# Kernel optimization log

Hardware: AMD Instinct MI355X
Metric: run time of the kernel (lower is better)

The kernel has to match this reference:

```python
import jax, jax.numpy as jnp
import numpy as np

B, NV, RN, SN = 1, 4, 1024, 128
H = W = 256
C_FEAT = 32   # img_feat_dim
D_VIEW = 32   # view transformer d_model
PE_D = 8      # PE_d_hid
D_RAY = D_VIEW + PE_D  # 40
NHEAD = 8
EPS_LN = 1e-5


def _layernorm(x, g, b):
    m = x.mean(-1, keepdims=True)
    v = ((x - m) ** 2).mean(-1, keepdims=True)
    return (x - m) * jax.lax.rsqrt(v + EPS_LN) * g + b


def _linear_attention(q, k, v):
    # LoFTR kernelized linear attention; q,k,v: (n, L, h, d)
    Q = jax.nn.elu(q) + 1.0
    K = jax.nn.elu(k) + 1.0
    L = v.shape[1]
    KV = jnp.einsum('nshd,nshv->nhdv', K, v / L)
    Z = 1.0 / (jnp.einsum('nlhd,nhd->nlh', Q, K.sum(axis=1)) + 1e-6)
    return jnp.einsum('nlhd,nhdv,nlh->nlhv', Q, KV, Z) * L


def _loftr_self_layer(x, Wq, Wk, Wv, Wm, g1, b1, W1, W2, g2, b2):
    # LoFTREncoderLayer with self-attention (x is both query and source)
    n, L, d = x.shape
    dim = d // NHEAD
    q = (x @ Wq).reshape(n, L, NHEAD, dim)
    k = (x @ Wk).reshape(n, L, NHEAD, dim)
    v = (x @ Wv).reshape(n, L, NHEAD, dim)
    msg = _linear_attention(q, k, v).reshape(n, L, d) @ Wm
    msg = _layernorm(msg, g1, b1)
    msg = jax.nn.relu(jnp.concatenate([x, msg], -1) @ W1) @ W2
    msg = _layernorm(msg, g2, b2)
    return x + msg


def _grid_sample_2d(img, pix):
    # img: (N,C,H,W); pix: (N,RN,SN,2) in pixel coords.
    # bilinear, align_corners=True, zero padding; mask = in-bounds.
    N, C, Hh, Ww = img.shape
    x, y = pix[..., 0], pix[..., 1]
    mask = ((x >= 0) & (x <= Ww - 1) & (y >= 0) & (y <= Hh - 1)).astype(img.dtype)
    x0 = jnp.floor(x)
    y0 = jnp.floor(y)
    flat = img.reshape(N, C, Hh * Ww)

    def gather(ix, iy):
        valid = ((ix >= 0) & (ix < Ww) & (iy >= 0) & (iy < Hh)).astype(img.dtype)
        idx = (jnp.clip(iy, 0, Hh - 1) * Ww + jnp.clip(ix, 0, Ww - 1)).astype(jnp.int32)
        out = jnp.take_along_axis(flat, idx.reshape(N, 1, -1), axis=2)
        return out.reshape(N, C, ix.shape[1], ix.shape[2]) * valid[:, None]

    wx1 = x - x0
    wy1 = y - y0
    out = (gather(x0, y0) * ((1 - wx1) * (1 - wy1))[:, None]
           + gather(x0 + 1, y0) * (wx1 * (1 - wy1))[:, None]
           + gather(x0, y0 + 1) * ((1 - wx1) * wy1)[:, None]
           + gather(x0 + 1, y0 + 1) * (wx1 * wy1)[:, None])
    return out, mask


def _order_posenc(d_hid, n):
    pos = np.arange(n)[:, None].astype(np.float64)
    j = np.arange(d_hid)[None, :]
    tab = pos / np.power(10000.0, 2 * (j // 2) / d_hid)
    tab[:, 0::2] = np.sin(tab[:, 0::2])
    tab[:, 1::2] = np.cos(tab[:, 1::2])
    return jnp.asarray(tab, dtype=jnp.float32)


def _forward(point3D, source_imgs, source_imgs_feat, ref_pose_inv, source_poses_inv,
             source_poses, view_token,
             vt_Wq, vt_Wk, vt_Wv, vt_Wm, vt_g1, vt_b1, vt_W1, vt_W2, vt_g2, vt_b2,
             rt_Wq, rt_Wk, rt_Wv, rt_Wm, rt_g1, rt_b1, rt_W1, rt_W2, rt_g2, rt_b2,
             dm_W1, dm_b1, dm_W2, dm_b2, dm_W3, dm_b3,
             rw_W1, rw_b1, rw_W2, rw_b2, rw_W3, rw_b3):
    b, nv, _, h, w = source_imgs.shape
    _, rn, sn, _ = point3D.shape

    # relative viewing directions (B,NV,RN,SN,3)
    v1 = point3D - ref_pose_inv[:, None, None, :3, -1]
    v2 = point3D[:, None] - source_poses_inv[:, :, None, None, :3, -1]
    v1 = v1 / jnp.linalg.norm(v1, axis=-1, keepdims=True)
    v2 = v2 / jnp.linalg.norm(v2, axis=-1, keepdims=True)
    dir_relative = v1[:, None] - v2

    # project points into all source views: (B,NV,3,RN,SN)
    pts_h = jnp.concatenate([point3D, jnp.ones_like(point3D[..., :1])], -1)
    pip = jnp.einsum('bnij,brsj->bnirs', source_poses, pts_h)[:, :, :3]
    mask_valid_depth = (pip[:, :, 2] > 0).astype(point3D.dtype)
    pix = pip[:, :, :2] / pip[:, :, 2:3]
    grid = jnp.moveaxis(pix, 2, -1).reshape(b * nv, rn, sn, 2)

    feat_s, mask = _grid_sample_2d(source_imgs_feat.reshape(b * nv, -1, h, w), grid)
    rgb_s, _ = _grid_sample_2d(source_imgs.reshape(b * nv, -1, h, w), grid)
    mask = mask.reshape(b, nv, rn, sn) * mask_valid_depth

    # per-point multi-view tokens: (B*RN*SN, NV, C)
    x = feat_s.reshape(b, nv, -1, rn, sn).transpose(0, 3, 4, 1, 2).reshape(b * rn * sn, nv, -1)
    tok = jnp.broadcast_to(view_token, (x.shape[0], 1, view_token.shape[-1]))
    x = jnp.concatenate([tok, x], axis=1)  # prepend view token -> L = NV+1
    x = _loftr_self_layer(x, vt_Wq, vt_Wk, vt_Wv, vt_Wm, vt_g1, vt_b1, vt_W1, vt_W2, vt_g2, vt_b2)

    x1 = jnp.moveaxis(x, 1, 0)          # (NV+1, B*RN*SN, C)
    view_feature = x1[1:]
    x = x1[0].reshape(b * rn, sn, -1)   # token output per sample along ray

    pe = _order_posenc(PE_D, sn)        # (SN, 8)
    x = jnp.concatenate([x, jnp.broadcast_to(pe, (b * rn, sn, PE_D))], -1)
    x = _loftr_self_layer(x, rt_Wq, rt_Wk, rt_Wv, rt_Wm, rt_g1, rt_b1, rt_W1, rt_W2, rt_g2, rt_b2)

    hdm = jax.nn.relu(x @ dm_W1 + dm_b1)
    hdm = jax.nn.relu(hdm @ dm_W2 + dm_b2)
    srdf = hdm @ dm_W3 + dm_b3           # (B*RN, SN, 1)

    # radiance blending weights over views
    vf = view_feature.reshape(nv, b, rn, sn, -1).transpose(1, 2, 3, 0, 4)  # (B,RN,SN,NV,C)
    dr = dir_relative.transpose(0, 2, 3, 1, 4)                             # (B,RN,SN,NV,3)
    xw = jnp.concatenate([vf, dr], -1)
    xw = jax.nn.relu(xw @ rw_W1 + rw_b1)
    xw = jax.nn.relu(xw @ rw_W2 + rw_b2)
    xw = xw @ rw_W3 + rw_b3                                                # (B,RN,SN,NV,1)
    m = mask.transpose(0, 2, 3, 1)[..., None]
    xw = jnp.where(m == 0, -1e9, xw)
    weight = jax.nn.softmax(xw, axis=-2)
    w_bn = weight[..., 0].transpose(0, 3, 1, 2)[:, :, None]                # (B,NV,1,RN,SN)
    radiance = (rgb_s.reshape(b, nv, 3, rn, sn) * w_bn).sum(axis=1)        # (B,3,RN,SN)
    radiance = radiance.transpose(0, 2, 3, 1).reshape(b * rn * sn, 3)
    return radiance, srdf, pip


def setup_inputs() -> dict:
    key = jax.random.key(0)
    ks = jax.random.split(key, 4)
    u = jax.random.uniform(ks[0], (B, RN, SN, 3), dtype=jnp.float32)
    point3D = jnp.concatenate([u[..., :2] - 0.5, u[..., 2:] + 1.0], -1)  # x,y in [-.5,.5], z in [1,2]
    source_imgs = jax.random.normal(ks[1], (B, NV, 3, H, W), dtype=jnp.float32) * 0.5
    source_imgs_feat = jax.random.normal(ks[2], (B, NV, C_FEAT, H, W), dtype=jnp.float32) * 0.5

    f = 200.0
    P = np.array([[f, 0, W / 2, 0], [0, f, H / 2, 0], [0, 0, 1, 0], [0, 0, 0, 1]], np.float32)
    source_poses = jnp.asarray(np.broadcast_to(P, (B, NV, 4, 4)).copy())
    ref_pose_inv = jnp.asarray(np.broadcast_to(np.eye(4, dtype=np.float32), (B, 4, 4)).copy())
    spi = np.broadcast_to(np.eye(4, dtype=np.float32), (B, NV, 4, 4)).copy()
    spi[:, :, 0, 3] = np.linspace(-0.2, 0.2, NV, dtype=np.float32)  # camera centers
    source_poses_inv = jnp.asarray(spi)

    pk = jax.random.split(ks[3], 20)

    def lin(k, i, o):
        return jax.random.normal(k, (i, o), dtype=jnp.float32) * 0.05

    d, dr = D_VIEW, D_RAY
    params = dict(
        view_token=jax.random.normal(pk[0], (1, d), dtype=jnp.float32),
        vt_Wq=lin(pk[1], d, d), vt_Wk=lin(pk[2], d, d), vt_Wv=lin(pk[3], d, d), vt_Wm=lin(pk[4], d, d),
        vt_g1=jnp.ones(d), vt_b1=jnp.zeros(d),
        vt_W1=lin(pk[5], 2 * d, 2 * d), vt_W2=lin(pk[6], 2 * d, d),
        vt_g2=jnp.ones(d), vt_b2=jnp.zeros(d),
        rt_Wq=lin(pk[7], dr, dr), rt_Wk=lin(pk[8], dr, dr), rt_Wv=lin(pk[9], dr, dr), rt_Wm=lin(pk[10], dr, dr),
        rt_g1=jnp.ones(dr), rt_b1=jnp.zeros(dr),
        rt_W1=lin(pk[11], 2 * dr, 2 * dr), rt_W2=lin(pk[12], 2 * dr, dr),
        rt_g2=jnp.ones(dr), rt_b2=jnp.zeros(dr),
        dm_W1=lin(pk[13], dr, 32), dm_b1=jnp.zeros(32),
        dm_W2=lin(pk[14], 32, 16), dm_b2=jnp.zeros(16),
        dm_W3=lin(pk[15], 16, 1), dm_b3=jnp.zeros(1),
        rw_W1=lin(pk[16], d + 3, 16), rw_b1=jnp.zeros(16),
        rw_W2=lin(pk[17], 16, 8), rw_b2=jnp.zeros(8),
        rw_W3=lin(pk[18], 8, 1), rw_b3=jnp.zeros(1),
    )
    out = dict(point3D=point3D, source_imgs=source_imgs, source_imgs_feat=source_imgs_feat,
               ref_pose_inv=ref_pose_inv, source_poses_inv=source_poses_inv,
               source_poses=source_poses)
    out.update(params)
    return out


def reference(point3D, source_imgs, source_imgs_feat, ref_pose_inv, source_poses_inv,
              source_poses, view_token,
              vt_Wq, vt_Wk, vt_Wv, vt_Wm, vt_g1, vt_b1, vt_W1, vt_W2, vt_g2, vt_b2,
              rt_Wq, rt_Wk, rt_Wv, rt_Wm, rt_g1, rt_b1, rt_W1, rt_W2, rt_g2, rt_b2,
              dm_W1, dm_b1, dm_W2, dm_b2, dm_W3, dm_b3,
              rw_W1, rw_b1, rw_W2, rw_b2, rw_W3, rw_b3):
    return _forward(point3D, source_imgs, source_imgs_feat, ref_pose_inv, source_poses_inv,
                    source_poses, view_token,
                    vt_Wq, vt_Wk, vt_Wv, vt_Wm, vt_g1, vt_b1, vt_W1, vt_W2, vt_g2, vt_b2,
                    rt_Wq, rt_Wk, rt_Wv, rt_Wm, rt_g1, rt_b1, rt_W1, rt_W2, rt_g2, rt_b2,
                    dm_W1, dm_b1, dm_W2, dm_b2, dm_W3, dm_b3,
                    rw_W1, rw_b1, rw_W2, rw_b2, rw_W3, rw_b3)
```

## Files before the change

### kernel.cpp

```cpp
#include <hip/hip_runtime.h>
#include <math.h>

#define NPTS   131072
#define NVIEW  4
#define IMH    256
#define IMW    256

#define WS_FEATT   0u
#define WS_IMGT    8388608u
#define WS_X1      9437184u
#define WS_XR      26214400u
#define WS_MSG     31457280u
#define WS_RGB     36700160u
#define WS_DIR     38273024u
#define WS_MASK    39845888u

__device__ __forceinline__ float elup1(float t) { return t > 0.f ? t + 1.f : expf(t); }

__global__ __launch_bounds__(256) void k0_transpose(
    const float* __restrict__ feat, const float* __restrict__ img,
    float* __restrict__ featT, float* __restrict__ imgT)
{
    int tid = blockIdx.x * 256 + threadIdx.x;
    int v = tid >> 16, pix = tid & 65535;
    float buf[32];
#pragma unroll
    for (int c = 0; c < 32; ++c)
        buf[c] = feat[((size_t)(v * 32 + c) << 16) + pix];
    float4* dst = (float4*)(featT + ((size_t)tid << 5));
#pragma unroll
    for (int q = 0; q < 8; ++q)
        dst[q] = make_float4(buf[4*q], buf[4*q+1], buf[4*q+2], buf[4*q+3]);
    float4 rgb;
    rgb.x = img[((size_t)(v * 3 + 0) << 16) + pix];
    rgb.y = img[((size_t)(v * 3 + 1) << 16) + pix];
    rgb.z = img[((size_t)(v * 3 + 2) << 16) + pix];
    rgb.w = 0.f;
    *(float4*)(imgT + ((size_t)tid << 2)) = rgb;
}

__global__ __launch_bounds__(256) void k1_geom_sample(
    const float* __restrict__ p3d, const float* __restrict__ rpi,
    const float* __restrict__ spi, const float* __restrict__ sp,
    const float* __restrict__ featT, const float* __restrict__ imgT,
    float* __restrict__ x1, float* __restrict__ rgbw,
    float* __restrict__ dirw, float* __restrict__ maskw,
    float* __restrict__ outpip)
{
    int tid = blockIdx.x * 256 + threadIdx.x;
    int p = tid >> 2, v = tid & 3;
    float X = p3d[p * 3 + 0], Y = p3d[p * 3 + 1], Z = p3d[p * 3 + 2];

    float a0 = X - rpi[3], a1 = Y - rpi[7], a2 = Z - rpi[11];
    float na = sqrtf(a0 * a0 + a1 * a1 + a2 * a2);
    a0 /= na; a1 /= na; a2 /= na;
    const float* sv = spi + v * 16;
    float b0 = X - sv[3], b1 = Y - sv[7], b2 = Z - sv[11];
    float nb = sqrtf(b0 * b0 + b1 * b1 + b2 * b2);
    b0 /= nb; b1 /= nb; b2 /= nb;
    dirw[(size_t)p * 12 + v * 3 + 0] = a0 - b0;
    dirw[(size_t)p * 12 + v * 3 + 1] = a1 - b1;
    dirw[(size_t)p * 12 + v * 3 + 2] = a2 - b2;

    const float* P = sp + v * 16;
    float pip0 = P[0] * X + P[1] * Y + P[2]  * Z + P[3];
    float pip1 = P[4] * X + P[5] * Y + P[6]  * Z + P[7];
    float pip2 = P[8] * X + P[9] * Y + P[10] * Z + P[11];
    outpip[(size_t)(v * 3 + 0) * NPTS + p] = pip0;
    outpip[(size_t)(v * 3 + 1) * NPTS + p] = pip1;
    outpip[(size_t)(v * 3 + 2) * NPTS + p] = pip2;

    float gx = pip0 / pip2, gy = pip1 / pip2;
    float inb = (gx >= 0.f && gx <= 255.f && gy >= 0.f && gy <= 255.f) ? 1.f : 0.f;
    float mvd = pip2 > 0.f ? 1.f : 0.f;
    maskw[(size_t)p * 4 + v] = inb * mvd;

    float x0f = floorf(gx), y0f = floorf(gy);
    float wx = gx - x0f, wy = gy - y0f;
    int ix0 = (int)x0f, iy0 = (int)y0f;
    float tw[4] = { (1.f-wx)*(1.f-wy), wx*(1.f-wy), (1.f-wx)*wy, wx*wy };
    int tdx[4] = { 0, 1, 0, 1 };
    int tdy[4] = { 0, 0, 1, 1 };

    float facc[32];
#pragma unroll
    for (int c = 0; c < 32; ++c) facc[c] = 0.f;
    float r0 = 0.f, r1 = 0.f, r2 = 0.f;

#pragma unroll
    for (int tno = 0; tno < 4; ++tno) {
        int ix = ix0 + tdx[tno], iy = iy0 + tdy[tno];
        float valid = (ix >= 0 && ix < IMW && iy >= 0 && iy < IMH) ? 1.f : 0.f;
        int cx = min(max(ix, 0), IMW - 1), cy = min(max(iy, 0), IMH - 1);
        float wgt = tw[tno] * valid;
        size_t base = ((size_t)v << 16) + ((size_t)cy << 8) + (size_t)cx;
        const float4* fp = (const float4*)(featT + base * 32);
#pragma unroll
        for (int q = 0; q < 8; ++q) {
            float4 f4 = fp[q];
            facc[4*q+0] += f4.x * wgt; facc[4*q+1] += f4.y * wgt;
            facc[4*q+2] += f4.z * wgt; facc[4*q+3] += f4.w * wgt;
        }
        float4 rp = *(const float4*)(imgT + base * 4);
        r0 += rp.x * wgt; r1 += rp.y * wgt; r2 += rp.z * wgt;
    }

    float4* xd = (float4*)(x1 + ((size_t)p * 4 + v) * 32);
#pragma unroll
    for (int q = 0; q < 8; ++q)
        xd[q] = make_float4(facc[4*q], facc[4*q+1], facc[4*q+2], facc[4*q+3]);
    rgbw[(size_t)p * 12 + v * 3 + 0] = r0;
    rgbw[(size_t)p * 12 + v * 3 + 1] = r1;
    rgbw[(size_t)p * 12 + v * 3 + 2] = r2;
}

#define K2_BLK    128
#define K2_PTS    24
#define K2_GRID   512
#define K2_NGRP   ((NPTS + K2_PTS - 1) / K2_PTS)

#define WQo   0
#define WKo   1024
#define WVo   2048
#define WMo   3072
#define W1o   4096
#define W2o   8192
#define LNo   10240

__device__ __forceinline__ void fma4(const float4 xv, const float* __restrict__ w,
                                     const int stride, float* __restrict__ acc)
{
#pragma unroll
    for (int j = 0; j < 32; ++j) acc[j] = fmaf(xv.x, w[j],            acc[j]);
#pragma unroll
    for (int j = 0; j < 32; ++j) acc[j] = fmaf(xv.y, w[stride + j],   acc[j]);
#pragma unroll
    for (int j = 0; j < 32; ++j) acc[j] = fmaf(xv.z, w[2*stride + j], acc[j]);
#pragma unroll
    for (int j = 0; j < 32; ++j) acc[j] = fmaf(xv.w, w[3*stride + j], acc[j]);
}

__global__ __launch_bounds__(K2_BLK) void k2_loftr1(
    float* __restrict__ x1g, const float* __restrict__ vtok,
    const float* __restrict__ Wq, const float* __restrict__ Wk,
    const float* __restrict__ Wv, const float* __restrict__ Wm,
    const float* __restrict__ g1v, const float* __restrict__ b1v,
    const float* __restrict__ W1, const float* __restrict__ W2,
    const float* __restrict__ g2v, const float* __restrict__ b2v,
    float* __restrict__ xr)
{
    __shared__ float wsm[10368];
    __shared__ float shr[8192];

    int t = threadIdx.x;
    for (int i = t; i < 1024; i += K2_BLK) {
        wsm[WQo + i] = Wq[i]; wsm[WKo + i] = Wk[i];
        wsm[WVo + i] = Wv[i]; wsm[WMo + i] = Wm[i];
    }
    for (int i = t; i < 4096; i += K2_BLK) wsm[W1o + i] = W1[i];
    for (int i = t; i < 2048; i += K2_BLK) wsm[W2o + i] = W2[i];
    if (t < 32) {
        wsm[LNo + t] = g1v[t]; wsm[LNo + 32 + t] = b1v[t];
        wsm[LNo + 64 + t] = g2v[t]; wsm[LNo + 96 + t] = b2v[t];
    }
    __syncthreads();

    int pl = t / 5, l = t - pl * 5;
    bool act = (t < K2_PTS * 5);
    if (!act) { pl = 0; l = 0; }
    const int rowbase = (pl * 5 + l) * 68;

    for (int grp = blockIdx.x; grp < K2_NGRP; grp += gridDim.x) {
        int p = grp * K2_PTS + pl;
        bool valid = act && (p < NPTS);
        int pload = p < NPTS ? p : NPTS - 1;
        const float4* xsrc = (l == 0) ? (const float4*)vtok
                                      : (const float4*)(x1g + ((size_t)pload * 4 + (l - 1)) * 32);

        __syncthreads();

        {
            float acc[32];
#pragma unroll
            for (int j = 0; j < 32; ++j) acc[j] = 0.f;
            for (int g = 0; g < 8; ++g) {
                float4 xv = xsrc[g];
                fma4(xv, &wsm[WKo + g * 128], 32, acc);
            }
            if (act) {
                float* krow = &shr[rowbase];
#pragma unroll
                for (int j = 0; j < 32; j += 4)
                    *(float4*)&krow[j] = make_float4(elup1(acc[j]), elup1(acc[j+1]),
                                                     elup1(acc[j+2]), elup1(acc[j+3]));
            }
        }
        {
            float acc[32];
#pragma unroll
            for (int j = 0; j < 32; ++j) acc[j] = 0.f;
            for (int g = 0; g < 8; ++g) {
                float4 xv = xsrc[g];
                fma4(xv, &wsm[WVo + g * 128], 32, acc);
            }
            if (act) {
                float* vrow = &shr[rowbase + 32];
#pragma unroll
                for (int j = 0; j < 32; j += 4)
                    *(float4*)&vrow[j] = make_float4(acc[j], acc[j+1], acc[j+2], acc[j+3]);
            }
        }
        __syncthreads();

        float macc[32];
#pragma unroll
        for (int j = 0; j < 32; ++j) macc[j] = 0.f;
        for (int h = 0; h < 8; ++h) {
            float q0 = 0.f, q1 = 0.f, q2 = 0.f, q3 = 0.f;
            for (int g = 0; g < 8; ++g) {
                float4 xv = xsrc[g];
                const float* w = &wsm[WQo + g * 128 + h * 4];
                q0 = fmaf(xv.x, w[0],  q0); q1 = fmaf(xv.x, w[1],  q1);
                q2 = fmaf(xv.x, w[2],  q2); q3 = fmaf(xv.x, w[3],  q3);
                q0 = fmaf(xv.y, w[32], q0); q1 = fmaf(xv.y, w[33], q1);
                q2 = fmaf(xv.y, w[34], q2); q3 = fmaf(xv.y, w[35], q3);
                q0 = fmaf(xv.z, w[64], q0); q1 = fmaf(xv.z, w[65], q1);
                q2 = fmaf(xv.z, w[66], q2); q3 = fmaf(xv.z, w[67], q3);
                q0 = fmaf(xv.w, w[96], q0); q1 = fmaf(xv.w, w[97], q1);
                q2 = fmaf(xv.w, w[98], q2); q3 = fmaf(xv.w, w[99], q3);
            }
            q0 = elup1(q0); q1 = elup1(q1); q2 = elup1(q2); q3 = elup1(q3);

            float kvm[16] = {0,0,0,0,0,0,0,0,0,0,0,0,0,0,0,0};
            float ks0 = 0.f, ks1 = 0.f, ks2 = 0.f, ks3 = 0.f;
#pragma unroll
            for (int l2 = 0; l2 < 5; ++l2) {
                const float* row = &shr[(pl * 5 + l2) * 68 + h * 4];
                float4 K4 = *(const float4*)row;
                float4 V4 = *(const float4*)(row + 32);
                kvm[0]  = fmaf(K4.x, V4.x, kvm[0]);  kvm[1]  = fmaf(K4.x, V4.y, kvm[1]);
                kvm[2]  = fmaf(K4.x, V4.z, kvm[2]);  kvm[3]  = fmaf(K4.x, V4.w, kvm[3]);
                kvm[4]  = fmaf(K4.y, V4.x, kvm[4]);  kvm[5]  = fmaf(K4.y, V4.y, kvm[5]);
                kvm[6]  = fmaf(K4.y, V4.z, kvm[6]);  kvm[7]  = fmaf(K4.y, V4.w, kvm[7]);
                kvm[8]  = fmaf(K4.z, V4.x, kvm[8]);  kvm[9]  = fmaf(K4.z, V4.y, kvm[9]);
                kvm[10] = fmaf(K4.z, V4.z, kvm[10]); kvm[11] = fmaf(K4.z, V4.w, kvm[11]);
                kvm[12] = fmaf(K4.w, V4.x, kvm[12]); kvm[13] = fmaf(K4.w, V4.y, kvm[13]);
                kvm[14] = fmaf(K4.w, V4.z, kvm[14]); kvm[15] = fmaf(K4.w, V4.w, kvm[15]);
                ks0 += K4.x; ks1 += K4.y; ks2 += K4.z; ks3 += K4.w;
            }
            float den = 1e-6f + q0*ks0 + q1*ks1 + q2*ks2 + q3*ks3;
            float inv = 1.f / den;
            float o0 = (q0*kvm[0] + q1*kvm[4] + q2*kvm[8]  + q3*kvm[12]) * inv;
            float o1 = (q0*kvm[1] + q1*kvm[5] + q2*kvm[9]  + q3*kvm[13]) * inv;
            float o2 = (q0*kvm[2] + q1*kvm[6] + q2*kvm[10] + q3*kvm[14]) * inv;
            float o3 = (q0*kvm[3] + q1*kvm[7] + q2*kvm[11] + q3*kvm[15]) * inv;

            const float* wm = &wsm[WMo + h * 4 * 32];
#pragma unroll
            for (int j = 0; j < 32; ++j) macc[j] = fmaf(o0, wm[j],      macc[j]);
#pragma unroll
            for (int j = 0; j < 32; ++j) macc[j] = fmaf(o1, wm[32 + j], macc[j]);
#pragma unroll
            for (int j = 0; j < 32; ++j) macc[j] = fmaf(o2, wm[64 + j], macc[j]);
#pragma unroll
            for (int j = 0; j < 32; ++j) macc[j] = fmaf(o3, wm[96 + j], macc[j]);
        }

        float msg[32];
        {
            float s1 = 0.f, s2 = 0.f;
#pragma unroll
            for (int j = 0; j < 32; ++j) { s1 += macc[j]; s2 += macc[j] * macc[j]; }
            float m  = s1 * (1.f / 32.f);
            float va = s2 * (1.f / 32.f) - m * m;
            float rs = rsqrtf(va + 1e-5f);
#pragma unroll
            for (int j = 0; j < 32; ++j)
                msg[j] = (macc[j] - m) * rs * wsm[LNo + j] + wsm[LNo + 32 + j];
        }
        __syncthreads();

#pragma unroll
        for (int g = 0; g < 8; ++g)
            *(float4*)&shr[(g * K2_BLK + t) * 4] =
                make_float4(msg[4*g], msg[4*g+1], msg[4*g+2], msg[4*g+3]);

        float oacc[32];
#pragma unroll
        for (int j = 0; j < 32; ++j) oacc[j] = 0.f;
        for (int half = 0; half < 2; ++half) {
            const int j0 = half * 32;
            float hacc[32];
#pragma unroll
            for (int j = 0; j < 32; ++j) hacc[j] = 0.f;
            for (int g = 0; g < 8; ++g) {
                float4 xv = xsrc[g];
                fma4(xv, &wsm[W1o + (g * 4) * 64 + j0], 64, hacc);
            }
            for (int g = 0; g < 8; ++g) {
                float4 mv = *(const float4*)&shr[(g * K2_BLK + t) * 4];
                fma4(mv, &wsm[W1o + (32 + g * 4) * 64 + j0], 64, hacc);
            }
#pragma unroll
            for (int j = 0; j < 32; j += 4)
                *(float4*)&shr[4096 + ((j >> 2) * K2_BLK + t) * 4] =
                    make_float4(fmaxf(hacc[j], 0.f),   fmaxf(hacc[j+1], 0.f),
                                fmaxf(hacc[j+2], 0.f), fmaxf(hacc[j+3], 0.f));
            for (int g = 0; g < 8; ++g) {
                float4 hv = *(const float4*)&shr[4096 + (g * K2_BLK + t) * 4];
                fma4(hv, &wsm[W2o + (j0 + g * 4) * 32], 32, oacc);
            }
        }

        {
            float s1 = 0.f, s2 = 0.f;
#pragma unroll
            for (int j = 0; j < 32; ++j) { s1 += oacc[j]; s2 += oacc[j] * oacc[j]; }
            float m  = s1 * (1.f / 32.f);
            float va = s2 * (1.f / 32.f) - m * m;
            float rs = rsqrtf(va + 1e-5f);

            if (valid) {
                float y[32];
#pragma unroll
                for (int g = 0; g < 8; ++g) {
                    float4 x4 = xsrc[g];
                    y[4*g] = x4.x; y[4*g+1] = x4.y; y[4*g+2] = x4.z; y[4*g+3] = x4.w;
                }
#pragma unroll
                for (int j = 0; j < 32; ++j)
                    y[j] += (oacc[j] - m) * rs * wsm[LNo + 64 + j] + wsm[LNo + 96 + j];

                if (l == 0) {
                    float4* dst = (float4*)(xr + (size_t)p * 40);
#pragma unroll
                    for (int g = 0; g < 8; ++g)
                        dst[g] = make_float4(y[4*g], y[4*g+1], y[4*g+2], y[4*g+3]);
                    int sidx = p & 127;
#pragma unroll
                    for (int c = 0; c < 8; ++c) {
                        float den = (c < 2) ? 1.f : (c < 4) ? 10.f : (c < 6) ? 100.f : 1000.f;
                        float arg = (float)sidx / den;
                        xr[(size_t)p * 40 + 32 + c] = (c & 1) ? cosf(arg) : sinf(arg);
                    }
                } else {
                    float4* dst = (float4*)(x1g + ((size_t)p * 4 + (l - 1)) * 32);
#pragma unroll
                    for (int g = 0; g < 8; ++g)
                        dst[g] = make_float4(y[4*g], y[4*g+1], y[4*g+2], y[4*g+3]);
                }
            }
        }
    }
}

__global__ __launch_bounds__(320) void k3a_attn(
    const float* __restrict__ xr,
    const float* __restrict__ Wq, const float* __restrict__ Wk,
    const float* __restrict__ Wv, const float* __restrict__ Wm,
    const float* __restrict__ g1, const float* __restrict__ b1,
    float* __restrict__ msg)
{
    __shared__ float kb[5120];
    __shared__ float vb[5120];
    __shared__ float wb[1600];
    __shared__ float kvb[200];
    __shared__ float ksb[40];
    int t = threadIdx.x, r = blockIdx.x;
    const float* xbase = xr + (size_t)r * 5120;
    int lg = t / 40, c = t % 40;

    for (int i = t; i < 1600; i += 320) wb[i] = Wk[i];
    __syncthreads();
    {
        float acc[16];
#pragma unroll
        for (int i = 0; i < 16; ++i) acc[i] = 0.f;
        for (int kk = 0; kk < 40; ++kk) {
            float w = wb[kk * 40 + c];
#pragma unroll
            for (int i = 0; i < 16; ++i) acc[i] += xbase[(lg * 16 + i) * 40 + kk] * w;
        }
#pragma unroll
        for (int i = 0; i < 16; ++i) kb[(lg * 16 + i) * 40 + c] = elup1(acc[i]);
    }
    __syncthreads();
    for (int i = t; i < 1600; i += 320) wb[i] = Wv[i];
    __syncthreads();
    {
        float acc[16];
#pragma unroll
        for (int i = 0; i < 16; ++i) acc[i] = 0.f;
        for (int kk = 0; kk < 40; ++kk) {
            float w = wb[kk * 40 + c];
#pragma unroll
            for (int i = 0; i < 16; ++i) acc[i] += xbase[(lg * 16 + i) * 40 + kk] * w;
        }
#pragma unroll
        for (int i = 0; i < 16; ++i) vb[(lg * 16 + i) * 40 + c] = acc[i];
    }
    __syncthreads();
    if (t < 200) {
        int h = t / 25, e = (t / 5) % 5, d = t % 5;
        float kv = 0.f, ks = 0.f;
        for (int s2 = 0; s2 < 128; ++s2) {
            float kvv = kb[s2 * 40 + h * 5 + e];
            float vv  = vb[s2 * 40 + h * 5 + d];
            kv += kvv * vv; ks += kvv;
        }
        kvb[t] = kv;
        if (d == 0) ksb[h * 5 + e] = ks;
    }
    __syncthreads();
    for (int i = t; i < 1600; i += 320) wb[i] = Wq[i];
    __syncthreads();
    {
        float acc[16];
#pragma unroll
        for (int i = 0; i < 16; ++i) acc[i] = 0.f;
        for (int kk = 0; kk < 40; ++kk) {
            float w = wb[kk * 40 + c];
#pragma unroll
            for (int i = 0; i < 16; ++i) acc[i] += xbase[(lg * 16 + i) * 40 + kk] * w;
        }
#pragma unroll
        for (int i = 0; i < 16; ++i) kb[(lg * 16 + i) * 40 + c] = elup1(acc[i]);
    }
    __syncthreads();
    {
        int h = c / 5, d = c % 5;
#pragma unroll 4
        for (int i = 0; i < 16; ++i) {
            int l = lg * 16 + i;
            float den = 1e-6f, o = 0.f;
#pragma unroll
            for (int e = 0; e < 5; ++e) {
                float q = kb[l * 40 + h * 5 + e];
                den += q * ksb[h * 5 + e];
                o   += q * kvb[h * 25 + e * 5 + d];
            }
            vb[l * 40 + c] = o / den;
        }
    }
    __syncthreads();
    for (int i = t; i < 1600; i += 320) wb[i] = Wm[i];
    __syncthreads();
    {
        float acc[16];
#pragma unroll
        for (int i = 0; i < 16; ++i) acc[i] = 0.f;
        for (int kk = 0; kk < 40; ++kk) {
            float w = wb[kk * 40 + c];
#pragma unroll
            for (int i = 0; i < 16; ++i) acc[i] += vb[(lg * 16 + i) * 40 + kk] * w;
        }
#pragma unroll
        for (int i = 0; i < 16; ++i) kb[(lg * 16 + i) * 40 + c] = acc[i];
    }
    __syncthreads();
    if (t < 128) {
        float s1 = 0.f, s2v = 0.f;
        for (int j = 0; j < 40; ++j) { float x = kb[t * 40 + j]; s1 += x; s2v += x * x; }
        float m = s1 * (1.f / 40.f), va = s2v * (1.f / 40.f) - m * m;
        float rs = rsqrtf(va + 1e-5f);
        for (int j = 0; j < 40; ++j)
            msg[((size_t)r * 128 + t) * 40 + j] = (kb[t * 40 + j] - m) * rs * g1[j] + b1[j];
    }
}

__global__ __launch_bounds__(320) void k3b_ffn(
    float* __restrict__ xr, const float* __restrict__ msg,
    const float* __restrict__ W1, const float* __restrict__ W2,
    const float* __restrict__ g2, const float* __restrict__ b2)
{
    __shared__ float hb[10240];
    __shared__ float wb[3200];
    int t = threadIdx.x, r = blockIdx.x;
    int lg = t / 40, c = t % 40;
    const float* xbase = xr + (size_t)r * 5120;
    const float* mbase = msg + (size_t)r * 5120;

    float hA[16], hB[16];
#pragma unroll
    for (int i = 0; i < 16; ++i) { hA[i] = 0.f; hB[i] = 0.f; }

    for (int i = t; i < 3200; i += 320) wb[i] = W1[i];
    __syncthreads();
    for (int kk = 0; kk < 40; ++kk) {
        float wa = wb[kk * 80 + c], wbb = wb[kk * 80 + c + 40];
#pragma unroll
        for (int i = 0; i < 16; ++i) {
            float xv = xbase[(lg * 16 + i) * 40 + kk];
            hA[i] += xv * wa; hB[i] += xv * wbb;
        }
    }
    __syncthreads();
    for (int i = t; i < 3200; i += 320) wb[i] = W1[3200 + i];
    __syncthreads();
    for (int kk = 0; kk < 40; ++kk) {
        float wa = wb[kk * 80 + c], wbb = wb[kk * 80 + c + 40];
#pragma unroll
        for (int i = 0; i < 16; ++i) {
            float mv = mbase[(lg * 16 + i) * 40 + kk];
            hA[i] += mv * wa; hB[i] += mv * wbb;
        }
    }
#pragma unroll
    for (int i = 0; i < 16; ++i) {
        hb[(lg * 16 + i) * 80 + c]      = fmaxf(hA[i], 0.f);
        hb[(lg * 16 + i) * 80 + c + 40] = fmaxf(hB[i], 0.f);
    }
    __syncthreads();
    for (int i = t; i < 3200; i += 320) wb[i] = W2[i];
    __syncthreads();
    float oa[16];
#pragma unroll
    for (int i = 0; i < 16; ++i) oa[i] = 0.f;
    for (int kk = 0; kk < 80; ++kk) {
        float w = wb[kk * 40 + c];
#pragma unroll
        for (int i = 0; i < 16; ++i) oa[i] += hb[(lg * 16 + i) * 80 + kk] * w;
    }
    __syncthreads();
#pragma unroll
    for (int i = 0; i < 16; ++i) hb[(lg * 16 + i) * 40 + c] = oa[i];
    __syncthreads();
    if (t < 128) {
        float s1 = 0.f, s2v = 0.f;
        for (int j = 0; j < 40; ++j) { float x = hb[t * 40 + j]; s1 += x; s2v += x * x; }
        float m = s1 * (1.f / 40.f), va = s2v * (1.f / 40.f) - m * m;
        float rs = rsqrtf(va + 1e-5f);
        for (int j = 0; j < 40; ++j) {
            float y = xbase[t * 40 + j] + (hb[t * 40 + j] - m) * rs * g2[j] + b2[j];
            xr[(size_t)r * 5120 + t * 40 + j] = y;
        }
    }
}

__global__ __launch_bounds__(256) void k4_dm(
    const float* __restrict__ xr,
    const float* __restrict__ W1, const float* __restrict__ b1,
    const float* __restrict__ W2, const float* __restrict__ b2,
    const float* __restrict__ W3, const float* __restrict__ b3,
    float* __restrict__ out1)
{
    __shared__ float s[1857];
    int t = threadIdx.x;
    for (int i = t; i < 1280; i += 256) s[i] = W1[i];
    if (t < 32) s[1280 + t] = b1[t];
    for (int i = t; i < 512; i += 256) s[1312 + i] = W2[i];
    if (t < 16) { s[1824 + t] = b2[t]; s[1840 + t] = W3[t]; }
    if (t == 0) s[1856] = b3[0];
    __syncthreads();

    int p = blockIdx.x * 256 + t;
    float x[40];
    const float4* xp = (const float4*)(xr + (size_t)p * 40);
#pragma unroll
    for (int i = 0; i < 10; ++i) {
        float4 v4 = xp[i];
        x[4*i] = v4.x; x[4*i+1] = v4.y; x[4*i+2] = v4.z; x[4*i+3] = v4.w;
    }
    float h1[32];
#pragma unroll
    for (int j = 0; j < 32; ++j) h1[j] = s[1280 + j];
    for (int k = 0; k < 40; ++k) {
        float xv = x[k];
#pragma unroll
        for (int j = 0; j < 32; ++j) h1[j] += xv * s[k * 32 + j];
    }
#pragma unroll
    for (int j = 0; j < 32; ++j) h1[j] = fmaxf(h1[j], 0.f);
    float h2[16];
#pragma unroll
    for (int j = 0; j < 16; ++j) h2[j] = s[1824 + j];
    for (int k = 0; k < 32; ++k) {
        float hv = h1[k];
#pragma unroll
        for (int j = 0; j < 16; ++j) h2[j] += hv * s[1312 + k * 16 + j];
    }
    float o = s[1856];
#pragma unroll
    for (int j = 0; j < 16; ++j) o += fmaxf(h2[j], 0.f) * s[1840 + j];
    out1[p] = o;
}

__global__ __launch_bounds__(256) void k5_rw(
    const float* __restrict__ vf, const float* __restrict__ dirw,
    const float* __restrict__ maskw, const float* __restrict__ rgbw,
    const float* __restrict__ W1, const float* __restrict__ b1,
    const float* __restrict__ W2, const float* __restrict__ b2,
    const float* __restrict__ W3, const float* __restrict__ b3,
    float* __restrict__ out0)
{
    __shared__ float s[721];
    int t = threadIdx.x;
    for (int i = t; i < 560; i += 256) s[i] = W1[i];
    if (t < 16) s[560 + t] = b1[t];
    if (t < 128) s[576 + t] = W2[t];
    if (t < 8) { s[704 + t] = b2[t]; s[712 + t] = W3[t]; }
    if (t == 0) s[720] = b3[0];
    __syncthreads();

    int p = blockIdx.x * 256 + t;
    float xw[4];
#pragma unroll
    for (int v = 0; v < 4; ++v) {
        float in[35];
        const float4* vp = (const float4*)(vf + ((size_t)p * 4 + v) * 32);
#pragma unroll
        for (int q = 0; q < 8; ++q) {
            float4 f4 = vp[q];
            in[4*q] = f4.x; in[4*q+1] = f4.y; in[4*q+2] = f4.z; in[4*q+3] = f4.w;
        }
        in[32] = dirw[(size_t)p * 12 + v * 3 + 0];
        in[33] = dirw[(size_t)p * 12 + v * 3 + 1];
        in[34] = dirw[(size_t)p * 12 + v * 3 + 2];
        float h1[16];
#pragma unroll
        for (int j = 0; j < 16; ++j) h1[j] = s[560 + j];
        for (int k = 0; k < 35; ++k) {
            float xv = in[k];
#pragma unroll
            for (int j = 0; j < 16; ++j) h1[j] += xv * s[k * 16 + j];
        }
        float h2[8];
#pragma unroll
        for (int j = 0; j < 8; ++j) h2[j] = s[704 + j];
        for (int k = 0; k < 16; ++k) {
            float hv = fmaxf(h1[k], 0.f);
#pragma unroll
            for (int j = 0; j < 8; ++j) h2[j] += hv * s[576 + k * 8 + j];
        }
        float o = s[720];
#pragma unroll
        for (int j = 0; j < 8; ++j) o += fmaxf(h2[j], 0.f) * s[712 + j];
        xw[v] = (maskw[(size_t)p * 4 + v] == 0.f) ? -1e9f : o;
    }
    float m = fmaxf(fmaxf(xw[0], xw[1]), fmaxf(xw[2], xw[3]));
    float e0 = expf(xw[0] - m), e1 = expf(xw[1] - m), e2 = expf(xw[2] - m), e3 = expf(xw[3] - m);
    float inv = 1.f / (e0 + e1 + e2 + e3);
    float w4[4] = { e0 * inv, e1 * inv, e2 * inv, e3 * inv };
    float r0 = 0.f, r1 = 0.f, r2 = 0.f;
#pragma unroll
    for (int v = 0; v < 4; ++v) {
        r0 += rgbw[(size_t)p * 12 + v * 3 + 0] * w4[v];
        r1 += rgbw[(size_t)p * 12 + v * 3 + 1] * w4[v];
        r2 += rgbw[(size_t)p * 12 + v * 3 + 2] * w4[v];
    }
    out0[(size_t)p * 3 + 0] = r0;
    out0[(size_t)p * 3 + 1] = r1;
    out0[(size_t)p * 3 + 2] = r2;
}

extern "C" void kernel_launch(void* const* d_in, const int* in_sizes, int n_in,
                              void* d_out, int out_size, void* d_ws, size_t ws_size,
                              hipStream_t stream) {
    (void)in_sizes; (void)n_in; (void)out_size; (void)ws_size;
    const float* p3d   = (const float*)d_in[0];
    const float* imgs  = (const float*)d_in[1];
    const float* feat  = (const float*)d_in[2];
    const float* rpi   = (const float*)d_in[3];
    const float* spi   = (const float*)d_in[4];
    const float* sp    = (const float*)d_in[5];
    const float* vtok  = (const float*)d_in[6];
    const float* vtWq  = (const float*)d_in[7];
    const float* vtWk  = (const float*)d_in[8];
    const float* vtWv  = (const float*)d_in[9];
    const float* vtWm  = (const float*)d_in[10];
    const float* vtg1  = (const float*)d_in[11];
    const float* vtb1  = (const float*)d_in[12];
    const float* vtW1  = (const float*)d_in[13];
    const float* vtW2  = (const float*)d_in[14];
    const float* vtg2  = (const float*)d_in[15];
    const float* vtb2  = (const float*)d_in[16];
    const float* rtWq  = (const float*)d_in[17];
    const float* rtWk  = (const float*)d_in[18];
    const float* rtWv  = (const float*)d_in[19];
    const float* rtWm  = (const float*)d_in[20];
    const float* rtg1  = (const float*)d_in[21];
    const float* rtb1  = (const float*)d_in[22];
    const float* rtW1  = (const float*)d_in[23];
    const float* rtW2  = (const float*)d_in[24];
    const float* rtg2  = (const float*)d_in[25];
    const float* rtb2  = (const float*)d_in[26];
    const float* dmW1  = (const float*)d_in[27];
    const float* dmb1  = (const float*)d_in[28];
    const float* dmW2  = (const float*)d_in[29];
    const float* dmb2  = (const float*)d_in[30];
    const float* dmW3  = (const float*)d_in[31];
    const float* dmb3  = (const float*)d_in[32];
    const float* rwW1  = (const float*)d_in[33];
    const float* rwb1  = (const float*)d_in[34];
    const float* rwW2  = (const float*)d_in[35];
    const float* rwb2  = (const float*)d_in[36];
    const float* rwW3  = (const float*)d_in[37];
    const float* rwb3  = (const float*)d_in[38];

    float* out  = (float*)d_out;
    float* out0 = out;
    float* out1 = out + 393216;
    float* out2 = out + 524288;

    float* ws    = (float*)d_ws;
    float* featT = ws + WS_FEATT;
    float* imgT  = ws + WS_IMGT;
    float* x1    = ws + WS_X1;
    float* xr    = ws + WS_XR;
    float* msg   = ws + WS_MSG;
    float* rgbw  = ws + WS_RGB;
    float* dirw  = ws + WS_DIR;
    float* maskw = ws + WS_MASK;

    k0_transpose<<<dim3(1024), dim3(256), 0, stream>>>(feat, imgs, featT, imgT);
    k1_geom_sample<<<dim3(2048), dim3(256), 0, stream>>>(p3d, rpi, spi, sp, featT, imgT,
                                                         x1, rgbw, dirw, maskw, out2);
    k2_loftr1<<<dim3(K2_GRID), dim3(K2_BLK), 0, stream>>>(x1, vtok, vtWq, vtWk, vtWv, vtWm,
                                                    vtg1, vtb1, vtW1, vtW2, vtg2, vtb2, xr);
    k3a_attn<<<dim3(1024), dim3(320), 0, stream>>>(xr, rtWq, rtWk, rtWv, rtWm, rtg1, rtb1, msg);
    k3b_ffn<<<dim3(1024), dim3(320), 0, stream>>>(xr, msg, rtW1, rtW2, rtg2, rtb2);
    k4_dm<<<dim3(512), dim3(256), 0, stream>>>(xr, dmW1, dmb1, dmW2, dmb2, dmW3, dmb3, out1);
    k5_rw<<<dim3(512), dim3(256), 0, stream>>>(x1, dirw, maskw, rgbw,
                                               rwW1, rwb1, rwW2, rwb2, rwW3, rwb3, out0);
}
```

Baseline: 1.162 ms.

## Split view-transformer layer into attention and FFN kernels with bf16 message buffer

```diff
diff --git a/kernel.cpp b/kernel.cpp
--- a/kernel.cpp
+++ b/kernel.cpp
@@ -1,4 +1,5 @@
 #include <hip/hip_runtime.h>
+#include <hip/hip_bf16.h>
 #include <math.h>
 
 #define NPTS   131072
@@ -14,8 +15,14 @@
 #define WS_RGB     36700160u
 #define WS_DIR     38273024u
 #define WS_MASK    39845888u
+#define WS_MSGV    40370176u
 
 __device__ __forceinline__ float elup1(float t) { return t > 0.f ? t + 1.f : expf(t); }
+
+__device__ __forceinline__ unsigned short f2bf(float f) {
+    __hip_bfloat16 h = __float2bfloat16(f);
+    return *(unsigned short*)&h;
+}
 
 __global__ __launch_bounds__(256) void k0_transpose(
     const float* __restrict__ feat, const float* __restrict__ img,
@@ -114,19 +121,6 @@
     rgbw[(size_t)p * 12 + v * 3 + 2] = r2;
 }
 
-#define K2_BLK    128
-#define K2_PTS    24
-#define K2_GRID   512
-#define K2_NGRP   ((NPTS + K2_PTS - 1) / K2_PTS)
-
-#define WQo   0
-#define WKo   1024
-#define WVo   2048
-#define WMo   3072
-#define W1o   4096
-#define W2o   8192
-#define LNo   10240
-
 __device__ __forceinline__ void fma4(const float4 xv, const float* __restrict__ w,
                                      const int stride, float* __restrict__ acc)
 {
@@ -140,217 +134,220 @@
     for (int j = 0; j < 32; ++j) acc[j] = fmaf(xv.w, w[3*stride + j], acc[j]);
 }
 
-__global__ __launch_bounds__(K2_BLK) void k2_loftr1(
-    float* __restrict__ x1g, const float* __restrict__ vtok,
+#define K2A_BLK  128
+#define K2A_PTS  24
+#define K2A_GRID ((NPTS + K2A_PTS - 1) / K2A_PTS)
+
+__global__ __launch_bounds__(K2A_BLK) void k2a_attn1(
+    const float* __restrict__ x1g, const float* __restrict__ vtok,
     const float* __restrict__ Wq, const float* __restrict__ Wk,
     const float* __restrict__ Wv, const float* __restrict__ Wm,
     const float* __restrict__ g1v, const float* __restrict__ b1v,
+    unsigned int* __restrict__ msgv)
+{
+    __shared__ float wsm[4160];
+    __shared__ float kv[8160];
+
+    int t = threadIdx.x;
+    for (int i = t; i < 1024; i += K2A_BLK) {
+        wsm[i] = Wq[i]; wsm[1024 + i] = Wk[i];
+        wsm[2048 + i] = Wv[i]; wsm[3072 + i] = Wm[i];
+    }
+    if (t < 32) { wsm[4096 + t] = g1v[t]; wsm[4128 + t] = b1v[t]; }
+    __syncthreads();
+
+    int pl = t / 5, l = t - pl * 5;
+    bool act = (t < K2A_PTS * 5);
+    if (!act) { pl = 0; l = 0; }
+    int p = blockIdx.x * K2A_PTS + pl;
+    bool valid = act && (p < NPTS);
+    int pload = p < NPTS ? p : NPTS - 1;
+    const float4* xsrc = (l == 0) ? (const float4*)vtok
+                                  : (const float4*)(x1g + ((size_t)pload * 4 + (l - 1)) * 32);
+    const int rowbase = (pl * 5 + l) * 68;
+
+    {
+        float acc[32];
+#pragma unroll
+        for (int j = 0; j < 32; ++j) acc[j] = 0.f;
+        for (int g = 0; g < 8; ++g) fma4(xsrc[g], &wsm[1024 + g * 128], 32, acc);
+        if (act) {
+            float* krow = &kv[rowbase];
+#pragma unroll
+            for (int j = 0; j < 32; j += 4)
+                *(float4*)&krow[j] = make_float4(elup1(acc[j]), elup1(acc[j+1]),
+                                                 elup1(acc[j+2]), elup1(acc[j+3]));
+        }
+    }
+    {
+        float acc[32];
+#pragma unroll
+        for (int j = 0; j < 32; ++j) acc[j] = 0.f;
+        for (int g = 0; g < 8; ++g) fma4(xsrc[g], &wsm[2048 + g * 128], 32, acc);
+        if (act) {
+            float* vrow = &kv[rowbase + 32];
+#pragma unroll
+            for (int j = 0; j < 32; j += 4)
+                *(float4*)&vrow[j] = make_float4(acc[j], acc[j+1], acc[j+2], acc[j+3]);
+        }
+    }
+    float qv[32];
+    {
+        float acc[32];
+#pragma unroll
+        for (int j = 0; j < 32; ++j) acc[j] = 0.f;
+        for (int g = 0; g < 8; ++g) fma4(xsrc[g], &wsm[g * 128], 32, acc);
+#pragma unroll
+        for (int j = 0; j < 32; ++j) qv[j] = elup1(acc[j]);
+    }
+    __syncthreads();
+
+    float macc[32];
+#pragma unroll
+    for (int j = 0; j < 32; ++j) macc[j] = 0.f;
+    for (int h = 0; h < 8; ++h) {
+        float kvm[16] = {0,0,0,0,0,0,0,0,0,0,0,0,0,0,0,0};
+        float ks0 = 0.f, ks1 = 0.f, ks2 = 0.f, ks3 = 0.f;
+#pragma unroll
+        for (int l2 = 0; l2 < 5; ++l2) {
+            const float* row = &kv[(pl * 5 + l2) * 68 + h * 4];
+            float4 K4 = *(const float4*)row;
+            float4 V4 = *(const float4*)(row + 32);
+            kvm[0]  = fmaf(K4.x, V4.x, kvm[0]);  kvm[1]  = fmaf(K4.x, V4.y, kvm[1]);
+            kvm[2]  = fmaf(K4.x, V4.z, kvm[2]);  kvm[3]  = fmaf(K4.x, V4.w, kvm[3]);
+            kvm[4]  = fmaf(K4.y, V4.x, kvm[4]);  kvm[5]  = fmaf(K4.y, V4.y, kvm[5]);
+            kvm[6]  = fmaf(K4.y, V4.z, kvm[6]);  kvm[7]  = fmaf(K4.y, V4.w, kvm[7]);
+            kvm[8]  = fmaf(K4.z, V4.x, kvm[8]);  kvm[9]  = fmaf(K4.z, V4.y, kvm[9]);
+            kvm[10] = fmaf(K4.z, V4.z, kvm[10]); kvm[11] = fmaf(K4.z, V4.w, kvm[11]);
+            kvm[12] = fmaf(K4.w, V4.x, kvm[12]); kvm[13] = fmaf(K4.w, V4.y, kvm[13]);
+            kvm[14] = fmaf(K4.w, V4.z, kvm[14]); kvm[15] = fmaf(K4.w, V4.w, kvm[15]);
+            ks0 += K4.x; ks1 += K4.y; ks2 += K4.z; ks3 += K4.w;
+        }
+        float q0 = qv[h*4], q1 = qv[h*4+1], q2 = qv[h*4+2], q3 = qv[h*4+3];
+        float den = 1e-6f + q0*ks0 + q1*ks1 + q2*ks2 + q3*ks3;
+        float inv = 1.f / den;
+        float o0 = (q0*kvm[0] + q1*kvm[4] + q2*kvm[8]  + q3*kvm[12]) * inv;
+        float o1 = (q0*kvm[1] + q1*kvm[5] + q2*kvm[9]  + q3*kvm[13]) * inv;
+        float o2 = (q0*kvm[2] + q1*kvm[6] + q2*kvm[10] + q3*kvm[14]) * inv;
+        float o3 = (q0*kvm[3] + q1*kvm[7] + q2*kvm[11] + q3*kvm[15]) * inv;
+
+        const float* wm = &wsm[3072 + h * 4 * 32];
+#pragma unroll
+        for (int j = 0; j < 32; ++j) macc[j] = fmaf(o0, wm[j],      macc[j]);
+#pragma unroll
+        for (int j = 0; j < 32; ++j) macc[j] = fmaf(o1, wm[32 + j], macc[j]);
+#pragma unroll
+        for (int j = 0; j < 32; ++j) macc[j] = fmaf(o2, wm[64 + j], macc[j]);
+#pragma unroll
+        for (int j = 0; j < 32; ++j) macc[j] = fmaf(o3, wm[96 + j], macc[j]);
+    }
+
+    if (valid) {
+        float s1 = 0.f, s2 = 0.f;
+#pragma unroll
+        for (int j = 0; j < 32; ++j) { s1 += macc[j]; s2 += macc[j] * macc[j]; }
+        float m  = s1 * (1.f / 32.f);
+        float va = s2 * (1.f / 32.f) - m * m;
+        float rs = rsqrtf(va + 1e-5f);
+        size_t tk = (size_t)p * 5 + l;
+        unsigned int* dst = msgv + tk * 16;
+#pragma unroll
+        for (int j = 0; j < 32; j += 2) {
+            float v0 = (macc[j]   - m) * rs * wsm[4096 + j]   + wsm[4128 + j];
+            float v1 = (macc[j+1] - m) * rs * wsm[4096 + j+1] + wsm[4128 + j+1];
+            dst[j >> 1] = ((unsigned int)f2bf(v1) << 16) | (unsigned int)f2bf(v0);
+        }
+    }
+}
+
+#define K2B_BLK  128
+#define K2B_GRID (NPTS * 5 / K2B_BLK)
+
+__global__ __launch_bounds__(K2B_BLK) void k2b_ffn1(
+    float* __restrict__ x1g, const float* __restrict__ vtok,
+    const unsigned int* __restrict__ msgv,
     const float* __restrict__ W1, const float* __restrict__ W2,
     const float* __restrict__ g2v, const float* __restrict__ b2v,
     float* __restrict__ xr)
 {
-    __shared__ float wsm[10368];
-    __shared__ float shr[8192];
-
+    __shared__ float wsm[6208];
     int t = threadIdx.x;
-    for (int i = t; i < 1024; i += K2_BLK) {
-        wsm[WQo + i] = Wq[i]; wsm[WKo + i] = Wk[i];
-        wsm[WVo + i] = Wv[i]; wsm[WMo + i] = Wm[i];
-    }
-    for (int i = t; i < 4096; i += K2_BLK) wsm[W1o + i] = W1[i];
-    for (int i = t; i < 2048; i += K2_BLK) wsm[W2o + i] = W2[i];
-    if (t < 32) {
-        wsm[LNo + t] = g1v[t]; wsm[LNo + 32 + t] = b1v[t];
-        wsm[LNo + 64 + t] = g2v[t]; wsm[LNo + 96 + t] = b2v[t];
-    }
-    __syncthreads();
-
-    int pl = t / 5, l = t - pl * 5;
-    bool act = (t < K2_PTS * 5);
-    if (!act) { pl = 0; l = 0; }
-    const int rowbase = (pl * 5 + l) * 68;
-
-    for (int grp = blockIdx.x; grp < K2_NGRP; grp += gridDim.x) {
-        int p = grp * K2_PTS + pl;
-        bool valid = act && (p < NPTS);
-        int pload = p < NPTS ? p : NPTS - 1;
-        const float4* xsrc = (l == 0) ? (const float4*)vtok
-                                      : (const float4*)(x1g + ((size_t)pload * 4 + (l - 1)) * 32);
-
-        __syncthreads();
-
-        {
-            float acc[32];
-#pragma unroll
-            for (int j = 0; j < 32; ++j) acc[j] = 0.f;
-            for (int g = 0; g < 8; ++g) {
-                float4 xv = xsrc[g];
-                fma4(xv, &wsm[WKo + g * 128], 32, acc);
-            }
-            if (act) {
-                float* krow = &shr[rowbase];
-#pragma unroll
-                for (int j = 0; j < 32; j += 4)
-                    *(float4*)&krow[j] = make_float4(elup1(acc[j]), elup1(acc[j+1]),
-                                                     elup1(acc[j+2]), elup1(acc[j+3]));
-            }
-        }
-        {
-            float acc[32];
-#pragma unroll
-            for (int j = 0; j < 32; ++j) acc[j] = 0.f;
-            for (int g = 0; g < 8; ++g) {
-                float4 xv = xsrc[g];
-                fma4(xv, &wsm[WVo + g * 128], 32, acc);
-            }
-            if (act) {
-                float* vrow = &shr[rowbase + 32];
-#pragma unroll
-                for (int j = 0; j < 32; j += 4)
-                    *(float4*)&vrow[j] = make_float4(acc[j], acc[j+1], acc[j+2], acc[j+3]);
-            }
-        }
-        __syncthreads();
-
-        float macc[32];
-#pragma unroll
-        for (int j = 0; j < 32; ++j) macc[j] = 0.f;
-        for (int h = 0; h < 8; ++h) {
-            float q0 = 0.f, q1 = 0.f, q2 = 0.f, q3 = 0.f;
-            for (int g = 0; g < 8; ++g) {
-                float4 xv = xsrc[g];
-                const float* w = &wsm[WQo + g * 128 + h * 4];
-                q0 = fmaf(xv.x, w[0],  q0); q1 = fmaf(xv.x, w[1],  q1);
-                q2 = fmaf(xv.x, w[2],  q2); q3 = fmaf(xv.x, w[3],  q3);
-                q0 = fmaf(xv.y, w[32], q0); q1 = fmaf(xv.y, w[33], q1);
-                q2 = fmaf(xv.y, w[34], q2); q3 = fmaf(xv.y, w[35], q3);
-                q0 = fmaf(xv.z, w[64], q0); q1 = fmaf(xv.z, w[65], q1);
-                q2 = fmaf(xv.z, w[66], q2); q3 = fmaf(xv.z, w[67], q3);
-                q0 = fmaf(xv.w, w[96], q0); q1 = fmaf(xv.w, w[97], q1);
-                q2 = fmaf(xv.w, w[98], q2); q3 = fmaf(xv.w, w[99], q3);
-            }
-            q0 = elup1(q0); q1 = elup1(q1); q2 = elup1(q2); q3 = elup1(q3);
-
-            float kvm[16] = {0,0,0,0,0,0,0,0,0,0,0,0,0,0,0,0};
-            float ks0 = 0.f, ks1 = 0.f, ks2 = 0.f, ks3 = 0.f;
-#pragma unroll
-            for (int l2 = 0; l2 < 5; ++l2) {
-                const float* row = &shr[(pl * 5 + l2) * 68 + h * 4];
-                float4 K4 = *(const float4*)row;
-                float4 V4 = *(const float4*)(row + 32);
-                kvm[0]  = fmaf(K4.x, V4.x, kvm[0]);  kvm[1]  = fmaf(K4.x, V4.y, kvm[1]);
-                kvm[2]  = fmaf(K4.x, V4.z, kvm[2]);  kvm[3]  = fmaf(K4.x, V4.w, kvm[3]);
-                kvm[4]  = fmaf(K4.y, V4.x, kvm[4]);  kvm[5]  = fmaf(K4.y, V4.y, kvm[5]);
-                kvm[6]  = fmaf(K4.y, V4.z, kvm[6]);  kvm[7]  = fmaf(K4.y, V4.w, kvm[7]);
-                kvm[8]  = fmaf(K4.z, V4.x, kvm[8]);  kvm[9]  = fmaf(K4.z, V4.y, kvm[9]);
-                kvm[10] = fmaf(K4.z, V4.z, kvm[10]); kvm[11] = fmaf(K4.z, V4.w, kvm[11]);
-                kvm[12] = fmaf(K4.w, V4.x, kvm[12]); kvm[13] = fmaf(K4.w, V4.y, kvm[13]);
-                kvm[14] = fmaf(K4.w, V4.z, kvm[14]); kvm[15] = fmaf(K4.w, V4.w, kvm[15]);
-                ks0 += K4.x; ks1 += K4.y; ks2 += K4.z; ks3 += K4.w;
-            }
-            float den = 1e-6f + q0*ks0 + q1*ks1 + q2*ks2 + q3*ks3;
-            float inv = 1.f / den;
-            float o0 = (q0*kvm[0] + q1*kvm[4] + q2*kvm[8]  + q3*kvm[12]) * inv;
-            float o1 = (q0*kvm[1] + q1*kvm[5] + q2*kvm[9]  + q3*kvm[13]) * inv;
-            float o2 = (q0*kvm[2] + q1*kvm[6] + q2*kvm[10] + q3*kvm[14]) * inv;
-            float o3 = (q0*kvm[3] + q1*kvm[7] + q2*kvm[11] + q3*kvm[15]) * inv;
-
-            const float* wm = &wsm[WMo + h * 4 * 32];
-#pragma unroll
-            for (int j = 0; j < 32; ++j) macc[j] = fmaf(o0, wm[j],      macc[j]);
-#pragma unroll
-            for (int j = 0; j < 32; ++j) macc[j] = fmaf(o1, wm[32 + j], macc[j]);
-#pragma unroll
-            for (int j = 0; j < 32; ++j) macc[j] = fmaf(o2, wm[64 + j], macc[j]);
-#pragma unroll
-            for (int j = 0; j < 32; ++j) macc[j] = fmaf(o3, wm[96 + j], macc[j]);
-        }
-
-        float msg[32];
-        {
-            float s1 = 0.f, s2 = 0.f;
-#pragma unroll
-            for (int j = 0; j < 32; ++j) { s1 += macc[j]; s2 += macc[j] * macc[j]; }
-            float m  = s1 * (1.f / 32.f);
-            float va = s2 * (1.f / 32.f) - m * m;
-            float rs = rsqrtf(va + 1e-5f);
-#pragma unroll
-            for (int j = 0; j < 32; ++j)
-                msg[j] = (macc[j] - m) * rs * wsm[LNo + j] + wsm[LNo + 32 + j];
-        }
-        __syncthreads();
-
-#pragma unroll
+    for (int i = t; i < 4096; i += K2B_BLK) wsm[i] = W1[i];
+    for (int i = t; i < 2048; i += K2B_BLK) wsm[4096 + i] = W2[i];
+    if (t < 32) { wsm[6144 + t] = g2v[t]; wsm[6176 + t] = b2v[t]; }
+    __syncthreads();
+
+    int tid = blockIdx.x * K2B_BLK + t;
+    int p = tid / 5, l = tid - p * 5;
+    const float4* xsrc = (l == 0) ? (const float4*)vtok
+                                  : (const float4*)(x1g + ((size_t)p * 4 + (l - 1)) * 32);
+    float x[32];
+#pragma unroll
+    for (int g = 0; g < 8; ++g) {
+        float4 v4 = xsrc[g];
+        x[4*g] = v4.x; x[4*g+1] = v4.y; x[4*g+2] = v4.z; x[4*g+3] = v4.w;
+    }
+    float msg[32];
+    {
+        const unsigned int* src = msgv + (size_t)tid * 16;
+#pragma unroll
+        for (int j = 0; j < 32; j += 2) {
+            unsigned int u = src[j >> 1];
+            msg[j]   = __uint_as_float(u << 16);
+            msg[j+1] = __uint_as_float(u & 0xffff0000u);
+        }
+    }
+
+    float oacc[32];
+#pragma unroll
+    for (int j = 0; j < 32; ++j) oacc[j] = 0.f;
+#pragma unroll
+    for (int half = 0; half < 2; ++half) {
+        const int j0 = half * 32;
+        float hacc[32];
+#pragma unroll
+        for (int j = 0; j < 32; ++j) hacc[j] = 0.f;
         for (int g = 0; g < 8; ++g)
-            *(float4*)&shr[(g * K2_BLK + t) * 4] =
-                make_float4(msg[4*g], msg[4*g+1], msg[4*g+2], msg[4*g+3]);
-
-        float oacc[32];
-#pragma unroll
-        for (int j = 0; j < 32; ++j) oacc[j] = 0.f;
-        for (int half = 0; half < 2; ++half) {
-            const int j0 = half * 32;
-            float hacc[32];
-#pragma unroll
-            for (int j = 0; j < 32; ++j) hacc[j] = 0.f;
-            for (int g = 0; g < 8; ++g) {
-                float4 xv = xsrc[g];
-                fma4(xv, &wsm[W1o + (g * 4) * 64 + j0], 64, hacc);
-            }
-            for (int g = 0; g < 8; ++g) {
-                float4 mv = *(const float4*)&shr[(g * K2_BLK + t) * 4];
-                fma4(mv, &wsm[W1o + (32 + g * 4) * 64 + j0], 64, hacc);
-            }
-#pragma unroll
-            for (int j = 0; j < 32; j += 4)
-                *(float4*)&shr[4096 + ((j >> 2) * K2_BLK + t) * 4] =
-                    make_float4(fmaxf(hacc[j], 0.f),   fmaxf(hacc[j+1], 0.f),
-                                fmaxf(hacc[j+2], 0.f), fmaxf(hacc[j+3], 0.f));
-            for (int g = 0; g < 8; ++g) {
-                float4 hv = *(const float4*)&shr[4096 + (g * K2_BLK + t) * 4];
-                fma4(hv, &wsm[W2o + (j0 + g * 4) * 32], 32, oacc);
-            }
-        }
-
-        {
-            float s1 = 0.f, s2 = 0.f;
-#pragma unroll
-            for (int j = 0; j < 32; ++j) { s1 += oacc[j]; s2 += oacc[j] * oacc[j]; }
-            float m  = s1 * (1.f / 32.f);
-            float va = s2 * (1.f / 32.f) - m * m;
-            float rs = rsqrtf(va + 1e-5f);
-
-            if (valid) {
-                float y[32];
-#pragma unroll
-                for (int g = 0; g < 8; ++g) {
-                    float4 x4 = xsrc[g];
-                    y[4*g] = x4.x; y[4*g+1] = x4.y; y[4*g+2] = x4.z; y[4*g+3] = x4.w;
-                }
-#pragma unroll
-                for (int j = 0; j < 32; ++j)
-                    y[j] += (oacc[j] - m) * rs * wsm[LNo + 64 + j] + wsm[LNo + 96 + j];
-
-                if (l == 0) {
-                    float4* dst = (float4*)(xr + (size_t)p * 40);
-#pragma unroll
-                    for (int g = 0; g < 8; ++g)
-                        dst[g] = make_float4(y[4*g], y[4*g+1], y[4*g+2], y[4*g+3]);
-                    int sidx = p & 127;
-#pragma unroll
-                    for (int c = 0; c < 8; ++c) {
-                        float den = (c < 2) ? 1.f : (c < 4) ? 10.f : (c < 6) ? 100.f : 1000.f;
-                        float arg = (float)sidx / den;
-                        xr[(size_t)p * 40 + 32 + c] = (c & 1) ? cosf(arg) : sinf(arg);
-                    }
-                } else {
-                    float4* dst = (float4*)(x1g + ((size_t)p * 4 + (l - 1)) * 32);
-#pragma unroll
-                    for (int g = 0; g < 8; ++g)
-                        dst[g] = make_float4(y[4*g], y[4*g+1], y[4*g+2], y[4*g+3]);
-                }
-            }
-        }
+            fma4(make_float4(x[4*g], x[4*g+1], x[4*g+2], x[4*g+3]),
+                 &wsm[(g * 4) * 64 + j0], 64, hacc);
+        for (int g = 0; g < 8; ++g)
+            fma4(make_float4(msg[4*g], msg[4*g+1], msg[4*g+2], msg[4*g+3]),
+                 &wsm[(32 + g * 4) * 64 + j0], 64, hacc);
+#pragma unroll
+        for (int j = 0; j < 32; ++j) hacc[j] = fmaxf(hacc[j], 0.f);
+        for (int g = 0; g < 8; ++g)
+            fma4(make_float4(hacc[4*g], hacc[4*g+1], hacc[4*g+2], hacc[4*g+3]),
+                 &wsm[4096 + (j0 + g * 4) * 32], 32, oacc);
+    }
+
+    float s1 = 0.f, s2 = 0.f;
+#pragma unroll
+    for (int j = 0; j < 32; ++j) { s1 += oacc[j]; s2 += oacc[j] * oacc[j]; }
+    float m  = s1 * (1.f / 32.f);
+    float va = s2 * (1.f / 32.f) - m * m;
+    float rs = rsqrtf(va + 1e-5f);
+    float y[32];
+#pragma unroll
+    for (int j = 0; j < 32; ++j)
+        y[j] = x[j] + (oacc[j] - m) * rs * wsm[6144 + j] + wsm[6176 + j];
+
+    if (l == 0) {
+        float4* dst = (float4*)(xr + (size_t)p * 40);
+#pragma unroll
+        for (int g = 0; g < 8; ++g)
+            dst[g] = make_float4(y[4*g], y[4*g+1], y[4*g+2], y[4*g+3]);
+        int sidx = p & 127;
+#pragma unroll
+        for (int c = 0; c < 8; ++c) {
+            float den = (c < 2) ? 1.f : (c < 4) ? 10.f : (c < 6) ? 100.f : 1000.f;
+            float arg = (float)sidx / den;
+            xr[(size_t)p * 40 + 32 + c] = (c & 1) ? cosf(arg) : sinf(arg);
+        }
+    } else {
+        float4* dst = (float4*)(x1g + ((size_t)p * 4 + (l - 1)) * 32);
+#pragma unroll
+        for (int g = 0; g < 8; ++g)
+            dst[g] = make_float4(y[4*g], y[4*g+1], y[4*g+2], y[4*g+3]);
     }
 }
 
@@ -402,13 +399,13 @@
     __syncthreads();
     if (t < 200) {
         int h = t / 25, e = (t / 5) % 5, d = t % 5;
-        float kv = 0.f, ks = 0.f;
+        float kvv2 = 0.f, ks = 0.f;
         for (int s2 = 0; s2 < 128; ++s2) {
             float kvv = kb[s2 * 40 + h * 5 + e];
             float vv  = vb[s2 * 40 + h * 5 + d];
-            kv += kvv * vv; ks += kvv;
-        }
-        kvb[t] = kv;
+            kvv2 += kvv * vv; ks += kvv;
+        }
+        kvb[t] = kvv2;
         if (d == 0) ksb[h * 5 + e] = ks;
     }
     __syncthreads();
@@ -711,12 +708,15 @@
     float* rgbw  = ws + WS_RGB;
     float* dirw  = ws + WS_DIR;
     float* maskw = ws + WS_MASK;
+    unsigned int* msgv = (unsigned int*)(ws + WS_MSGV);
 
     k0_transpose<<<dim3(1024), dim3(256), 0, stream>>>(feat, imgs, featT, imgT);
     k1_geom_sample<<<dim3(2048), dim3(256), 0, stream>>>(p3d, rpi, spi, sp, featT, imgT,
                                                          x1, rgbw, dirw, maskw, out2);
-    k2_loftr1<<<dim3(K2_GRID), dim3(K2_BLK), 0, stream>>>(x1, vtok, vtWq, vtWk, vtWv, vtWm,
-                                                    vtg1, vtb1, vtW1, vtW2, vtg2, vtb2, xr);
+    k2a_attn1<<<dim3(K2A_GRID), dim3(K2A_BLK), 0, stream>>>(x1, vtok, vtWq, vtWk, vtWv, vtWm,
+                                                            vtg1, vtb1, msgv);
+    k2b_ffn1<<<dim3(K2B_GRID), dim3(K2B_BLK), 0, stream>>>(x1, vtok, msgv, vtW1, vtW2,
+                                                           vtg2, vtb2, xr);
     k3a_attn<<<dim3(1024), dim3(320), 0, stream>>>(xr, rtWq, rtWk, rtWv, rtWm, rtg1, rtb1, msg);
     k3b_ffn<<<dim3(1024), dim3(320), 0, stream>>>(xr, msg, rtW1, rtW2, rtg2, rtb2);
     k4_dm<<<dim3(512), dim3(256), 0, stream>>>(xr, dmW1, dmb1, dmW2, dmb2, dmW3, dmb3, out1);
```

Result: slower. 1.206 ms (+3.8%).
